# Kernel optimization log

Measured on AMD Instinct MI355X. Metric: run time of the kernel, lower is better.

Reference implementation:

```python
import jax, jax.numpy as jnp
import numpy as np

N_NODES = 150000
N_EDGES = 2400000
N_GRAPHS = 1024
EPS = 1e-5


def setup_inputs() -> dict:
    key = jax.random.key(0)
    ks = jax.random.split(key, 20)
    x = jax.random.normal(ks[0], (N_NODES, 3), dtype=jnp.float32)
    edge_index = jax.random.randint(ks[1], (2, N_EDGES), 0, N_NODES, dtype=jnp.int64)
    batch = jnp.sort(jax.random.randint(ks[2], (N_NODES,), 0, N_GRAPHS, dtype=jnp.int64))

    def glorot(k, shape):
        fan_in, fan_out = shape[0], shape[1]
        lim = jnp.sqrt(6.0 / (fan_in + fan_out)).astype(jnp.float32)
        return jax.random.uniform(k, shape, jnp.float32, -lim, lim)

    params = dict(
        W1=glorot(ks[3], (3, 32)), b1=jnp.zeros((32,), jnp.float32),
        gn1_w=jnp.ones((32,), jnp.float32), gn1_b=jnp.zeros((32,), jnp.float32), gn1_ms=jnp.ones((32,), jnp.float32),
        W2=glorot(ks[4], (32, 32)), b2=jnp.zeros((32,), jnp.float32),
        gn2_w=jnp.ones((32,), jnp.float32), gn2_b=jnp.zeros((32,), jnp.float32), gn2_ms=jnp.ones((32,), jnp.float32),
        W3=glorot(ks[5], (32, 32)), b3=jnp.zeros((32,), jnp.float32),
        gn3_w=jnp.ones((32,), jnp.float32), gn3_b=jnp.zeros((32,), jnp.float32), gn3_ms=jnp.ones((32,), jnp.float32),
        lin_w=glorot(ks[6], (32, 3)), lin_b=jnp.zeros((3,), jnp.float32),
    )
    return dict(x=x, edge_index=edge_index, batch=batch, **params)


def _gcn_conv(x, W, b, src, dst, dinv_sqrt):
    # PyG GCNConv: h = x @ W; propagate with sym-normalized A + self-loops; + bias
    h = x @ W  # [N, F]
    coef = dinv_sqrt[src] * dinv_sqrt[dst]  # [E]
    msgs = h[src] * coef[:, None]  # [E, F]
    agg = jax.ops.segment_sum(msgs, dst, num_segments=N_NODES)
    agg = agg + (dinv_sqrt * dinv_sqrt)[:, None] * h  # self-loop term
    return agg + b


def _graph_norm(x, batch, counts, weight, bias, mean_scale):
    # PyG GraphNorm: per-graph mean/var with learnable mean_scale
    mean = jax.ops.segment_sum(x, batch, num_segments=N_GRAPHS) / counts[:, None]
    out = x - mean_scale * mean[batch]
    var = jax.ops.segment_sum(out * out, batch, num_segments=N_GRAPHS) / counts[:, None]
    std = jnp.sqrt(var + EPS)
    return weight * out / std[batch] + bias


def reference(x, edge_index, batch,
              W1, b1, gn1_w, gn1_b, gn1_ms,
              W2, b2, gn2_w, gn2_b, gn2_ms,
              W3, b3, gn3_w, gn3_b, gn3_ms,
              lin_w, lin_b):
    src, dst = edge_index[0], edge_index[1]
    # degree over A + I (edge weight 1)
    deg = jax.ops.segment_sum(jnp.ones((N_EDGES,), jnp.float32), dst, num_segments=N_NODES) + 1.0
    dinv_sqrt = jax.lax.rsqrt(deg)
    counts = jax.ops.segment_sum(jnp.ones((N_NODES,), jnp.float32), batch, num_segments=N_GRAPHS)

    x1 = jax.nn.relu(_graph_norm(_gcn_conv(x, W1, b1, src, dst, dinv_sqrt), batch, counts, gn1_w, gn1_b, gn1_ms))
    h2 = _graph_norm(_gcn_conv(x1, W2, b2, src, dst, dinv_sqrt), batch, counts, gn2_w, gn2_b, gn2_ms)
    x2 = jax.nn.relu(h2 + x1)
    h3 = _graph_norm(_gcn_conv(x2, W3, b3, src, dst, dinv_sqrt), batch, counts, gn3_w, gn3_b, gn3_ms)
    x3 = jax.nn.relu(h3 + x2)

    pooled = jax.ops.segment_sum(x3, batch, num_segments=N_GRAPHS) / counts[:, None]  # mean pool
    return pooled @ lin_w + lin_b  # [G, 3]
```

## Files before the change

### kernel.cpp

```cpp
#include <hip/hip_runtime.h>

#define N_NODES 150000
#define N_EDGES 2400000
#define N_GRAPHS 1024
#define F 32
#define EPSV 1e-5f

#define BS 256
#define NB ((N_NODES + BS - 1) / BS)
#define EB 8192
#define NEB ((N_EDGES + EB - 1) / EB)
#define EPT (EB / 256)

__device__ __forceinline__ float bflo(unsigned int u) {
    union { unsigned int i; float f; } v; v.i = u << 16; return v.f;
}
__device__ __forceinline__ float bfhi(unsigned int u) {
    union { unsigned int i; float f; } v; v.i = u & 0xffff0000u; return v.f;
}
__device__ __forceinline__ unsigned int f2bf(float f) {
    union { float f; unsigned int i; } v; v.f = f;
    unsigned int r = v.i + 0x7fff + ((v.i >> 16) & 1);
    return r >> 16;
}

__global__ void k_init(const int* __restrict__ batch, int* __restrict__ bucketCnt,
                       int* __restrict__ off, int* __restrict__ rowptr) {
    int i = blockIdx.x * blockDim.x + threadIdx.x;
    if (i >= N_NODES) return;
    if (i < NB) bucketCnt[i] = 0;
    if (i == 0) rowptr[N_NODES] = N_EDGES;
    int b = batch[i];
    if (i == 0) {
        for (int g = 0; g <= b; ++g) off[g] = 0;
    } else {
        int pb = batch[i - 1];
        for (int g = pb + 1; g <= b; ++g) off[g] = i;
    }
    if (i == N_NODES - 1) {
        for (int g = b + 1; g <= N_GRAPHS; ++g) off[g] = N_NODES;
    }
}

__global__ __launch_bounds__(256) void k_bhist(const int* __restrict__ dst,
                                               int* __restrict__ bucketCnt) {
    __shared__ int h[NB];
    int t = threadIdx.x;
    for (int b = t; b < NB; b += 256) h[b] = 0;
    __syncthreads();
    int base = blockIdx.x * EB + t;
#pragma unroll
    for (int k = 0; k < EPT; ++k) {
        int e = base + k * 256;
        if (e < N_EDGES) atomicAdd(&h[dst[e] >> 8], 1);
    }
    __syncthreads();
    for (int b = t; b < NB; b += 256) {
        int c = h[b];
        if (c) atomicAdd(&bucketCnt[b], c);
    }
}

__global__ __launch_bounds__(256) void k_bscan(const int* __restrict__ bucketCnt,
                                               int* __restrict__ bucketOff,
                                               int* __restrict__ bucketCur) {
    __shared__ int sc[256];
    int t = threadIdx.x;
    int v[3];
    int s = 0;
#pragma unroll
    for (int k = 0; k < 3; ++k) {
        int i = t * 3 + k;
        v[k] = (i < NB) ? bucketCnt[i] : 0;
        s += v[k];
    }
    sc[t] = s;
    __syncthreads();
    for (int o = 1; o < 256; o <<= 1) {
        int x = (t >= o) ? sc[t - o] : 0;
        __syncthreads();
        sc[t] += x;
        __syncthreads();
    }
    int run = sc[t] - s;
#pragma unroll
    for (int k = 0; k < 3; ++k) {
        int i = t * 3 + k;
        if (i < NB) { bucketOff[i] = run; bucketCur[i] = run; }
        run += v[k];
    }
    if (t == 0) bucketOff[NB] = N_EDGES;
}

__global__ __launch_bounds__(256) void k_bin(const int* __restrict__ src,
                                             const int* __restrict__ dst,
                                             int* __restrict__ bucketCur,
                                             unsigned int* __restrict__ binned) {
    __shared__ int h[NB];
    __shared__ int gb[NB];
    int t = threadIdx.x;
    for (int b = t; b < NB; b += 256) h[b] = 0;
    __syncthreads();
    int base = blockIdx.x * EB + t;
    unsigned int key[EPT];
    unsigned int pk[EPT];
#pragma unroll
    for (int k = 0; k < EPT; ++k) {
        int e = base + k * 256;
        if (e < N_EDGES) {
            int d = dst[e];
            int b = d >> 8;
            key[k] = ((unsigned int)(d & 255) << 18) | (unsigned int)src[e];
            unsigned int rk = (unsigned int)atomicAdd(&h[b], 1);
            pk[k] = (rk << 10) | (unsigned int)b;
        } else {
            pk[k] = 0xFFFFFFFFu;
        }
    }
    __syncthreads();
    for (int b = t; b < NB; b += 256) {
        int c = h[b];
        gb[b] = c ? atomicAdd(&bucketCur[b], c) : 0;
    }
    __syncthreads();
#pragma unroll
    for (int k = 0; k < EPT; ++k) {
        if (pk[k] != 0xFFFFFFFFu) {
            unsigned int b = pk[k] & 1023u;
            unsigned int rk = pk[k] >> 10;
            binned[gb[b] + rk] = key[k];
        }
    }
}

__global__ __launch_bounds__(256) void k_csr(const unsigned int* __restrict__ binned,
                                             const int* __restrict__ bucketOff,
                                             const float* __restrict__ x,
                                             int* __restrict__ rowptr,
                                             float* __restrict__ dinv,
                                             float* __restrict__ xs,
                                             int* __restrict__ csr) {
    __shared__ int lcnt[256];
    __shared__ int lpre[256];
    __shared__ int sc[256];
    int b = blockIdx.x, t = threadIdx.x;
    int e0 = bucketOff[b], e1 = bucketOff[b + 1];
    lcnt[t] = 0;
    __syncthreads();
    for (int e = e0 + t; e < e1; e += 256)
        atomicAdd(&lcnt[binned[e] >> 18], 1);
    __syncthreads();
    int v = lcnt[t];
    sc[t] = v;
    __syncthreads();
    for (int o = 1; o < 256; o <<= 1) {
        int x2 = (t >= o) ? sc[t - o] : 0;
        __syncthreads();
        sc[t] += x2;
        __syncthreads();
    }
    int excl = sc[t] - v;
    lpre[t] = excl;
    int gnode = b * BS + t;
    if (gnode < N_NODES) {
        rowptr[gnode] = e0 + excl;
        float dv = rsqrtf((float)v + 1.0f);
        dinv[gnode] = dv;
        xs[gnode * 3 + 0] = x[gnode * 3 + 0] * dv;
        xs[gnode * 3 + 1] = x[gnode * 3 + 1] * dv;
        xs[gnode * 3 + 2] = x[gnode * 3 + 2] * dv;
    }
    lcnt[t] = 0;
    __syncthreads();
    for (int e = e0 + t; e < e1; e += 256) {
        unsigned int key = binned[e];
        int ld = key >> 18;
        int pos = atomicAdd(&lcnt[ld], 1);
        csr[e0 + lpre[ld] + pos] = (int)(key & 0x3FFFFu);
    }
}

__global__ __launch_bounds__(256) void k_gat3(
        const float* __restrict__ xs, const int* __restrict__ csr,
        const int* __restrict__ rowptr, const float* __restrict__ dinv,
        const float* __restrict__ W, const float* __restrict__ bias,
        float* __restrict__ y) {
    int gid = blockIdx.x * 256 + threadIdx.x;
    int n = gid >> 3, c = gid & 7;
    if (n >= N_NODES) return;
    float z0 = xs[n * 3 + 0], z1 = xs[n * 3 + 1], z2 = xs[n * 3 + 2];
    int e0 = rowptr[n], e1 = rowptr[n + 1];
    for (int e = e0; e < e1; ++e) {
        int s = csr[e];
        z0 += xs[s * 3 + 0];
        z1 += xs[s * 3 + 1];
        z2 += xs[s * 3 + 2];
    }
    float dd = dinv[n];
    z0 *= dd; z1 *= dd; z2 *= dd;
    float4 w0 = ((const float4*)(W + 0 * F))[c];
    float4 w1 = ((const float4*)(W + 1 * F))[c];
    float4 w2 = ((const float4*)(W + 2 * F))[c];
    float4 o  = ((const float4*)bias)[c];
    o.x += z0 * w0.x + z1 * w1.x + z2 * w2.x;
    o.y += z0 * w0.y + z1 * w1.y + z2 * w2.y;
    o.z += z0 * w0.z + z1 * w1.z + z2 * w2.z;
    o.w += z0 * w0.w + z1 * w1.w + z2 * w2.w;
    ((float4*)y)[n * 8 + c] = o;
}

__global__ __launch_bounds__(256) void k_gat32(
        const unsigned short* __restrict__ xh, const int* __restrict__ csr,
        const int* __restrict__ rowptr, const float* __restrict__ dinv,
        const float* __restrict__ W, const float* __restrict__ bias,
        float* __restrict__ y) {
    __shared__ float Ws[F * F];
    __shared__ float bs[F];
    __shared__ float Zs[64 * 36];
    int t = threadIdx.x;
    ((float4*)Ws)[t] = ((const float4*)W)[t];
    if (t < F) bs[t] = bias[t];
    __syncthreads();

    int gid = blockIdx.x * 256 + t;
    int n = gid >> 2, c = gid & 3, ln = t >> 2;
    bool act = (n < N_NODES);
    float acc[8];
    if (act) {
        const uint4* xr = (const uint4*)xh;
        uint4 us = xr[n * 4 + c];
        acc[0] = bflo(us.x); acc[1] = bfhi(us.x);
        acc[2] = bflo(us.y); acc[3] = bfhi(us.y);
        acc[4] = bflo(us.z); acc[5] = bfhi(us.z);
        acc[6] = bflo(us.w); acc[7] = bfhi(us.w);
        int e0 = rowptr[n], e1 = rowptr[n + 1];
        int e = e0;
        for (; e + 3 < e1; e += 4) {
            int s0 = csr[e], s1 = csr[e + 1], s2 = csr[e + 2], s3 = csr[e + 3];
            uint4 u0 = xr[s0 * 4 + c];
            uint4 u1 = xr[s1 * 4 + c];
            uint4 u2 = xr[s2 * 4 + c];
            uint4 u3 = xr[s3 * 4 + c];
            acc[0] += bflo(u0.x); acc[1] += bfhi(u0.x);
            acc[2] += bflo(u0.y); acc[3] += bfhi(u0.y);
            acc[4] += bflo(u0.z); acc[5] += bfhi(u0.z);
            acc[6] += bflo(u0.w); acc[7] += bfhi(u0.w);
            acc[0] += bflo(u1.x); acc[1] += bfhi(u1.x);
            acc[2] += bflo(u1.y); acc[3] += bfhi(u1.y);
            acc[4] += bflo(u1.z); acc[5] += bfhi(u1.z);
            acc[6] += bflo(u1.w); acc[7] += bfhi(u1.w);
            acc[0] += bflo(u2.x); acc[1] += bfhi(u2.x);
            acc[2] += bflo(u2.y); acc[3] += bfhi(u2.y);
            acc[4] += bflo(u2.z); acc[5] += bfhi(u2.z);
            acc[6] += bflo(u2.w); acc[7] += bfhi(u2.w);
            acc[0] += bflo(u3.x); acc[1] += bfhi(u3.x);
            acc[2] += bflo(u3.y); acc[3] += bfhi(u3.y);
            acc[4] += bflo(u3.z); acc[5] += bfhi(u3.z);
            acc[6] += bflo(u3.w); acc[7] += bfhi(u3.w);
        }
        for (; e < e1; ++e) {
            int s0 = csr[e];
            uint4 u0 = xr[s0 * 4 + c];
            acc[0] += bflo(u0.x); acc[1] += bfhi(u0.x);
            acc[2] += bflo(u0.y); acc[3] += bfhi(u0.y);
            acc[4] += bflo(u0.z); acc[5] += bfhi(u0.z);
            acc[6] += bflo(u0.w); acc[7] += bfhi(u0.w);
        }
        float dd = dinv[n];
#pragma unroll
        for (int j = 0; j < 8; ++j) acc[j] *= dd;
    } else {
#pragma unroll
        for (int j = 0; j < 8; ++j) acc[j] = 0.f;
    }
    *(float4*)&Zs[ln * 36 + c * 8]     = *(float4*)&acc[0];
    *(float4*)&Zs[ln * 36 + c * 8 + 4] = *(float4*)&acc[4];
    __syncthreads();

    if (act) {
        const float* zrow = &Zs[ln * 36];
        float4 o0 = ((const float4*)bs)[c * 2];
        float4 o1 = ((const float4*)bs)[c * 2 + 1];
#pragma unroll
        for (int k = 0; k < F; ++k) {
            float zk = zrow[k];
            float4 w0 = ((const float4*)&Ws[k * F])[c * 2];
            float4 w1 = ((const float4*)&Ws[k * F])[c * 2 + 1];
            o0.x += zk * w0.x; o0.y += zk * w0.y; o0.z += zk * w0.z; o0.w += zk * w0.w;
            o1.x += zk * w1.x; o1.y += zk * w1.y; o1.z += zk * w1.z; o1.w += zk * w1.w;
        }
        ((float4*)y)[n * 8 + c * 2]     = o0;
        ((float4*)y)[n * 8 + c * 2 + 1] = o1;
    }
}

template <bool RES, bool WXH>
__global__ __launch_bounds__(256) void k_gn2(
        const float* agg, const float* res, const int* __restrict__ off,
        const float* __restrict__ gw, const float* __restrict__ gb,
        const float* __restrict__ gms, const float* __restrict__ dinv,
        unsigned short* __restrict__ xh, float* outp) {
    __shared__ float red1[256], red2[256];
    __shared__ float mv_s[F], sc_s[F];
    int g = blockIdx.x;
    int i0 = off[g], i1 = off[g + 1];
    float rc = 1.0f / (float)(i1 - i0);
    int t = threadIdx.x;
    int f = t & 31, r0 = t >> 5;

    float s = 0.f, q = 0.f;
    for (int n = i0 + r0; n < i1; n += 8) {
        float v = agg[n * F + f];
        s += v; q += v * v;
    }
    red1[t] = s; red2[t] = q; __syncthreads();
    if (t < 128) { red1[t] += red1[t + 128]; red2[t] += red2[t + 128]; } __syncthreads();
    if (t < 64)  { red1[t] += red1[t + 64];  red2[t] += red2[t + 64];  } __syncthreads();
    if (t < 32) {
        float sm = (red1[t] + red1[t + 32]) * rc;
        float sq = (red2[t] + red2[t + 32]) * rc;
        float mv = gms[t] * sm;
        float var = sq - mv * (2.f * sm - mv);
        mv_s[t] = mv;
        sc_s[t] = gw[t] * rsqrtf(var + EPSV);
    }
    __syncthreads();

    float w = sc_s[f], mv = mv_s[f], bb = gb[f];
    for (int n = i0 + r0; n < i1; n += 8) {
        float y = (agg[n * F + f] - mv) * w + bb;
        if (RES) y += res[n * F + f];
        y = fmaxf(y, 0.f);
        outp[n * F + f] = y;
        if (WXH) xh[n * F + f] = (unsigned short)f2bf(y * dinv[n]);
    }
}

__global__ __launch_bounds__(256) void k_gnfin(
        const float* __restrict__ agg, const float* __restrict__ res,
        const int* __restrict__ off,
        const float* __restrict__ gw, const float* __restrict__ gb,
        const float* __restrict__ gms,
        const float* __restrict__ lin_w, const float* __restrict__ lin_b,
        float* __restrict__ outp) {
    __shared__ float red1[256], red2[256];
    __shared__ float mv_s[F], sc_s[F], pooled_s[F];
    int g = blockIdx.x;
    int i0 = off[g], i1 = off[g + 1];
    float cnt = (float)(i1 - i0);
    float rc = 1.0f / cnt;
    int t = threadIdx.x;
    int f = t & 31, r0 = t >> 5;

    float s = 0.f, q = 0.f;
    for (int n = i0 + r0; n < i1; n += 8) {
        float v = agg[n * F + f];
        s += v; q += v * v;
    }
    red1[t] = s; red2[t] = q; __syncthreads();
    if (t < 128) { red1[t] += red1[t + 128]; red2[t] += red2[t + 128]; } __syncthreads();
    if (t < 64)  { red1[t] += red1[t + 64];  red2[t] += red2[t + 64];  } __syncthreads();
    if (t < 32) {
        float sm = (red1[t] + red1[t + 32]) * rc;
        float sq = (red2[t] + red2[t + 32]) * rc;
        float mv = gms[t] * sm;
        float var = sq - mv * (2.f * sm - mv);
        mv_s[t] = mv;
        sc_s[t] = gw[t] * rsqrtf(var + EPSV);
    }
    __syncthreads();

    float w = sc_s[f], mv = mv_s[f], bb = gb[f];
    float ps = 0.f;
    for (int n = i0 + r0; n < i1; n += 8) {
        float yv = (agg[n * F + f] - mv) * w + bb + res[n * F + f];
        ps += fmaxf(yv, 0.f);
    }
    __syncthreads();
    red1[t] = ps; __syncthreads();
    if (t < 128) red1[t] += red1[t + 128]; __syncthreads();
    if (t < 64)  red1[t] += red1[t + 64];  __syncthreads();
    if (t < 32) { red1[t] += red1[t + 32]; pooled_s[t] = red1[t] * rc; }
    __syncthreads();
    if (t < 3) {
        float o = lin_b[t];
#pragma unroll
        for (int f2 = 0; f2 < F; ++f2) o += pooled_s[f2] * lin_w[f2 * 3 + t];
        outp[g * 3 + t] = o;
    }
}

extern "C" void kernel_launch(void* const* d_in, const int* in_sizes, int n_in,
                              void* d_out, int out_size, void* d_ws, size_t ws_size,
                              hipStream_t stream) {
    const float* x      = (const float*)d_in[0];
    const int*   ei     = (const int*)d_in[1];
    const int*   batch  = (const int*)d_in[2];
    const float* W1     = (const float*)d_in[3];
    const float* b1     = (const float*)d_in[4];
    const float* gn1w   = (const float*)d_in[5];
    const float* gn1b   = (const float*)d_in[6];
    const float* gn1ms  = (const float*)d_in[7];
    const float* W2     = (const float*)d_in[8];
    const float* b2     = (const float*)d_in[9];
    const float* gn2w   = (const float*)d_in[10];
    const float* gn2b   = (const float*)d_in[11];
    const float* gn2ms  = (const float*)d_in[12];
    const float* W3     = (const float*)d_in[13];
    const float* b3     = (const float*)d_in[14];
    const float* gn3w   = (const float*)d_in[15];
    const float* gn3b   = (const float*)d_in[16];
    const float* gn3ms  = (const float*)d_in[17];
    const float* lin_w  = (const float*)d_in[18];
    const float* lin_b  = (const float*)d_in[19];
    float* out = (float*)d_out;

    const int* srcp = ei;
    const int* dstp = ei + N_EDGES;

    char* ws = (char*)d_ws;
    size_t p = 0;
    auto alloc = [&](size_t bytes) {
        size_t r = p; p += (bytes + 511) & ~(size_t)511; return r;
    };
    int*   off       = (int*)  (ws + alloc(sizeof(int) * (N_GRAPHS + 1)));
    int*   bucketCnt = (int*)  (ws + alloc(sizeof(int) * NB));
    int*   bucketOff = (int*)  (ws + alloc(sizeof(int) * (NB + 1)));
    int*   bucketCur = (int*)  (ws + alloc(sizeof(int) * NB));
    int*   rowptr    = (int*)  (ws + alloc(sizeof(int) * (N_NODES + 1)));
    float* dinv      = (float*)(ws + alloc(sizeof(float) * N_NODES));
    float* xs        = (float*)(ws + alloc(sizeof(float) * N_NODES * 3));
    unsigned int* binned = (unsigned int*)(ws + alloc(sizeof(unsigned int) * N_EDGES));
    int*   csr       = (int*)  (ws + alloc(sizeof(int) * N_EDGES));
    float* A         = (float*)(ws + alloc(sizeof(float) * N_NODES * F));
    float* B         = (float*)(ws + alloc(sizeof(float) * N_NODES * F));
    unsigned short* xh = (unsigned short*)binned;
    (void)ws_size; (void)n_in; (void)in_sizes; (void)out_size;

    const int TB = 256;
    dim3 blk(TB);
    int ngrid  = (N_NODES + TB - 1) / TB;
    int ggrid8 = (N_NODES * 8 + TB - 1) / TB;
    int ggrid4 = (N_NODES * 4 + TB - 1) / TB;

    k_init <<<ngrid, blk, 0, stream>>>(batch, bucketCnt, off, rowptr);
    k_bhist<<<NEB, blk, 0, stream>>>(dstp, bucketCnt);
    k_bscan<<<1, blk, 0, stream>>>(bucketCnt, bucketOff, bucketCur);
    k_bin  <<<NEB, blk, 0, stream>>>(srcp, dstp, bucketCur, binned);
    k_csr  <<<NB, blk, 0, stream>>>(binned, bucketOff, x, rowptr, dinv, xs, csr);

    k_gat3 <<<ggrid8, blk, 0, stream>>>(xs, csr, rowptr, dinv, W1, b1, A);
    k_gn2<false, true><<<N_GRAPHS, blk, 0, stream>>>(
        A, nullptr, off, gn1w, gn1b, gn1ms, dinv, xh, A);

    k_gat32<<<ggrid4, blk, 0, stream>>>(xh, csr, rowptr, dinv, W2, b2, B);
    k_gn2<true, true><<<N_GRAPHS, blk, 0, stream>>>(
        B, A, off, gn2w, gn2b, gn2ms, dinv, xh, B);

    k_gat32<<<ggrid4, blk, 0, stream>>>(xh, csr, rowptr, dinv, W3, b3, A);
    k_gnfin<<<N_GRAPHS, blk, 0, stream>>>(A, B, off, gn3w, gn3b, gn3ms,
                                          lin_w, lin_b, out);
}
```

Baseline: 338.5 us.

## Compute layer-1 GraphNorm stats from 3-dim aggregated features via second moments

Replaces the layer-1 gather and per-graph GraphNorm pass with three kernels. The first aggregates only the 3-dim normalized inputs once per node, with no 8x redundant gather, and accumulates per-graph first and second moments (9 values) through shared and global atomics. The second derives the 32-feature mean and variance analytically from those moments and W1. The third applies the linear map, normalization and ReLU and writes the bf16 copy, removing the separate GraphNorm read of the 32-wide activations. The E[y^2]-mean^2 variance form can lose precision, and the float atomics make results nondeterministic.

Result: no change. 332.7 us (-1.7%).

```diff
diff --git a/kernel.cpp b/kernel.cpp
--- a/kernel.cpp
+++ b/kernel.cpp
@@ -180,33 +180,118 @@
     }
 }
 
-__global__ __launch_bounds__(256) void k_gat3(
+__global__ __launch_bounds__(256) void k_gz(
         const float* __restrict__ xs, const int* __restrict__ csr,
         const int* __restrict__ rowptr, const float* __restrict__ dinv,
+        const int* __restrict__ batch,
+        float* __restrict__ zs, float* __restrict__ gstats) {
+    __shared__ float st[8 * 12];
+    __shared__ int gbase_s;
+    int t = threadIdx.x;
+    for (int i = t; i < 8 * 12; i += 256) st[i] = 0.f;
+    if (t == 0) gbase_s = batch[blockIdx.x * 256];
+    __syncthreads();
+
+    int n = blockIdx.x * 256 + t;
+    if (n < N_NODES) {
+        float z0 = xs[n * 3 + 0], z1 = xs[n * 3 + 1], z2 = xs[n * 3 + 2];
+        int e0 = rowptr[n], e1 = rowptr[n + 1];
+        for (int e = e0; e < e1; ++e) {
+            int s = csr[e];
+            z0 += xs[s * 3 + 0];
+            z1 += xs[s * 3 + 1];
+            z2 += xs[s * 3 + 2];
+        }
+        float dd = dinv[n];
+        z0 *= dd; z1 *= dd; z2 *= dd;
+        zs[n * 3 + 0] = z0; zs[n * 3 + 1] = z1; zs[n * 3 + 2] = z2;
+        int g = batch[n];
+        int lg = g - gbase_s;
+        if (lg < 8) {
+            float* sp = &st[lg * 12];
+            atomicAdd(&sp[0], z0);      atomicAdd(&sp[1], z1);
+            atomicAdd(&sp[2], z2);      atomicAdd(&sp[3], z0 * z0);
+            atomicAdd(&sp[4], z0 * z1); atomicAdd(&sp[5], z0 * z2);
+            atomicAdd(&sp[6], z1 * z1); atomicAdd(&sp[7], z1 * z2);
+            atomicAdd(&sp[8], z2 * z2);
+        } else {
+            float* gp = &gstats[g * 9];
+            atomicAdd(&gp[0], z0);      atomicAdd(&gp[1], z1);
+            atomicAdd(&gp[2], z2);      atomicAdd(&gp[3], z0 * z0);
+            atomicAdd(&gp[4], z0 * z1); atomicAdd(&gp[5], z0 * z2);
+            atomicAdd(&gp[6], z1 * z1); atomicAdd(&gp[7], z1 * z2);
+            atomicAdd(&gp[8], z2 * z2);
+        }
+    }
+    __syncthreads();
+    if (t < 72) {
+        int slot = t / 9, k = t % 9;
+        int g = gbase_s + slot;
+        float v = st[slot * 12 + k];
+        if (g < N_GRAPHS && v != 0.f) atomicAdd(&gstats[g * 9 + k], v);
+    }
+}
+
+__global__ __launch_bounds__(256) void k_prep(
+        const float* __restrict__ gstats, const int* __restrict__ off,
         const float* __restrict__ W, const float* __restrict__ bias,
-        float* __restrict__ y) {
+        const float* __restrict__ gw, const float* __restrict__ gb_unused,
+        const float* __restrict__ gms,
+        float* __restrict__ mvA, float* __restrict__ scA) {
+    int gid = blockIdx.x * 256 + threadIdx.x;
+    if (gid >= N_GRAPHS * F) return;
+    int g = gid >> 5, f = gid & 31;
+    float rc = 1.0f / (float)(off[g + 1] - off[g]);
+    const float* sp = &gstats[g * 9];
+    float S0 = sp[0], S1 = sp[1], S2 = sp[2];
+    float m00 = sp[3], m01 = sp[4], m02 = sp[5], m11 = sp[6], m12 = sp[7], m22 = sp[8];
+    float w0 = W[0 * F + f], w1 = W[1 * F + f], w2 = W[2 * F + f];
+    float b = bias[f];
+    float sy = w0 * S0 + w1 * S1 + w2 * S2;
+    float m = sy * rc + b;
+    float q = w0 * w0 * m00 + w1 * w1 * m11 + w2 * w2 * m22
+            + 2.f * (w0 * w1 * m01 + w0 * w2 * m02 + w1 * w2 * m12);
+    float Ey2 = q * rc + 2.f * b * (sy * rc) + b * b;
+    float mv = gms[f] * m;
+    float var = Ey2 - 2.f * mv * m + mv * mv;
+    mvA[gid] = mv;
+    scA[gid] = gw[f] * rsqrtf(var + EPSV);
+}
+
+__global__ __launch_bounds__(256) void k_n1(
+        const float* __restrict__ zs, const int* __restrict__ batch,
+        const float* __restrict__ dinv,
+        const float* __restrict__ W, const float* __restrict__ bias,
+        const float* __restrict__ gb,
+        const float* __restrict__ mvA, const float* __restrict__ scA,
+        unsigned short* __restrict__ xh, float* __restrict__ outp) {
     int gid = blockIdx.x * 256 + threadIdx.x;
     int n = gid >> 3, c = gid & 7;
     if (n >= N_NODES) return;
-    float z0 = xs[n * 3 + 0], z1 = xs[n * 3 + 1], z2 = xs[n * 3 + 2];
-    int e0 = rowptr[n], e1 = rowptr[n + 1];
-    for (int e = e0; e < e1; ++e) {
-        int s = csr[e];
-        z0 += xs[s * 3 + 0];
-        z1 += xs[s * 3 + 1];
-        z2 += xs[s * 3 + 2];
-    }
+    float z0 = zs[n * 3 + 0], z1 = zs[n * 3 + 1], z2 = zs[n * 3 + 2];
+    int g = batch[n];
     float dd = dinv[n];
-    z0 *= dd; z1 *= dd; z2 *= dd;
     float4 w0 = ((const float4*)(W + 0 * F))[c];
     float4 w1 = ((const float4*)(W + 1 * F))[c];
     float4 w2 = ((const float4*)(W + 2 * F))[c];
-    float4 o  = ((const float4*)bias)[c];
-    o.x += z0 * w0.x + z1 * w1.x + z2 * w2.x;
-    o.y += z0 * w0.y + z1 * w1.y + z2 * w2.y;
-    o.z += z0 * w0.z + z1 * w1.z + z2 * w2.z;
-    o.w += z0 * w0.w + z1 * w1.w + z2 * w2.w;
-    ((float4*)y)[n * 8 + c] = o;
+    float4 y  = ((const float4*)bias)[c];
+    y.x += z0 * w0.x + z1 * w1.x + z2 * w2.x;
+    y.y += z0 * w0.y + z1 * w1.y + z2 * w2.y;
+    y.z += z0 * w0.z + z1 * w1.z + z2 * w2.z;
+    y.w += z0 * w0.w + z1 * w1.w + z2 * w2.w;
+    float4 mv = ((const float4*)mvA)[g * 8 + c];
+    float4 sc = ((const float4*)scA)[g * 8 + c];
+    float4 bb = ((const float4*)gb)[c];
+    float4 o;
+    o.x = fmaxf((y.x - mv.x) * sc.x + bb.x, 0.f);
+    o.y = fmaxf((y.y - mv.y) * sc.y + bb.y, 0.f);
+    o.z = fmaxf((y.z - mv.z) * sc.z + bb.z, 0.f);
+    o.w = fmaxf((y.w - mv.w) * sc.w + bb.w, 0.f);
+    ((float4*)outp)[n * 8 + c] = o;
+    uint2 hp;
+    hp.x = f2bf(o.x * dd) | (f2bf(o.y * dd) << 16);
+    hp.y = f2bf(o.z * dd) | (f2bf(o.w * dd) << 16);
+    ((uint2*)xh)[n * 8 + c] = hp;
 }
 
 __global__ __launch_bounds__(256) void k_gat32(
@@ -430,6 +515,10 @@
     int*   rowptr    = (int*)  (ws + alloc(sizeof(int) * (N_NODES + 1)));
     float* dinv      = (float*)(ws + alloc(sizeof(float) * N_NODES));
     float* xs        = (float*)(ws + alloc(sizeof(float) * N_NODES * 3));
+    float* zs        = (float*)(ws + alloc(sizeof(float) * N_NODES * 3));
+    float* gstats    = (float*)(ws + alloc(sizeof(float) * N_GRAPHS * 9));
+    float* mvA       = (float*)(ws + alloc(sizeof(float) * N_GRAPHS * F));
+    float* scA       = (float*)(ws + alloc(sizeof(float) * N_GRAPHS * F));
     unsigned int* binned = (unsigned int*)(ws + alloc(sizeof(unsigned int) * N_EDGES));
     int*   csr       = (int*)  (ws + alloc(sizeof(int) * N_EDGES));
     float* A         = (float*)(ws + alloc(sizeof(float) * N_NODES * F));
@@ -443,15 +532,18 @@
     int ggrid8 = (N_NODES * 8 + TB - 1) / TB;
     int ggrid4 = (N_NODES * 4 + TB - 1) / TB;
 
+    hipMemsetAsync(gstats, 0, sizeof(float) * N_GRAPHS * 9, stream);
+
     k_init <<<ngrid, blk, 0, stream>>>(batch, bucketCnt, off, rowptr);
     k_bhist<<<NEB, blk, 0, stream>>>(dstp, bucketCnt);
     k_bscan<<<1, blk, 0, stream>>>(bucketCnt, bucketOff, bucketCur);
     k_bin  <<<NEB, blk, 0, stream>>>(srcp, dstp, bucketCur, binned);
     k_csr  <<<NB, blk, 0, stream>>>(binned, bucketOff, x, rowptr, dinv, xs, csr);
 
-    k_gat3 <<<ggrid8, blk, 0, stream>>>(xs, csr, rowptr, dinv, W1, b1, A);
-    k_gn2<false, true><<<N_GRAPHS, blk, 0, stream>>>(
-        A, nullptr, off, gn1w, gn1b, gn1ms, dinv, xh, A);
+    k_gz  <<<ngrid, blk, 0, stream>>>(xs, csr, rowptr, dinv, batch, zs, gstats);
+    k_prep<<<(N_GRAPHS * F + TB - 1) / TB, blk, 0, stream>>>(
+        gstats, off, W1, b1, gn1w, gn1b, gn1ms, mvA, scA);
+    k_n1  <<<ggrid8, blk, 0, stream>>>(zs, batch, dinv, W1, b1, gn1b, mvA, scA, xh, A);
 
     k_gat32<<<ggrid4, blk, 0, stream>>>(xh, csr, rowptr, dinv, W2, b2, B);
     k_gn2<true, true><<<N_GRAPHS, blk, 0, stream>>>(
```
